# Optimization experiments

Hardware: AMD Instinct MI355X
Metric: run time of the kernel (lower is better)

The kernel has to match this reference:

```python
import jax, jax.numpy as jnp
import numpy as np

EPS = 1e-5

def setup_inputs() -> dict:
    key = jax.random.key(0)
    k1, k2, k3, k4, k5 = jax.random.split(key, 5)
    b, n, e, c = 256, 257, 768, 1
    x = jax.random.normal(k1, (b, n, e), dtype=jnp.float32)
    ln_gamma = jnp.ones((e,), dtype=jnp.float32)
    ln_beta = jnp.zeros((e,), dtype=jnp.float32)
    # nn.Linear default init: uniform(-1/sqrt(e), 1/sqrt(e))
    bound = 1.0 / np.sqrt(e)
    W = jax.random.uniform(k2, (c, e), dtype=jnp.float32, minval=-bound, maxval=bound)
    bias = jax.random.uniform(k3, (c,), dtype=jnp.float32, minval=-bound, maxval=bound)
    return {"x": x, "ln_gamma": ln_gamma, "ln_beta": ln_beta, "W": W, "bias": bias}

def reference(x, ln_gamma, ln_beta, W, bias):
    # drop CLS token: [b, n-1, e]
    h = x[:, 1:, :]
    mu = jnp.mean(h, axis=-1, keepdims=True)
    var = jnp.mean(jnp.square(h - mu), axis=-1, keepdims=True)
    h = (h - mu) * jax.lax.rsqrt(var + EPS) * ln_gamma + ln_beta
    # linear: [b, n-1, c]
    logits = jnp.einsum('bne,ce->bnc', h, W) + bias
    return jax.nn.sigmoid(logits)
```

## Files before the change

### kernel.cpp

```cpp
#include <hip/hip_runtime.h>
#include <hip/hip_bf16.h>

#define EPS 1e-5f

__global__ __launch_bounds__(256) void prep_kernel(
    const float* __restrict__ g, const float* __restrict__ beta,
    const float* __restrict__ W, const float* __restrict__ bias,
    float* __restrict__ gw, float* __restrict__ consts) {
    int t = threadIdx.x;
    float sgw = 0.f, sbw = 0.f;
    for (int i = t; i < 768; i += 256) {
        float gv = g[i] * W[i];
        gw[i] = gv;
        sgw += gv;
        sbw += beta[i] * W[i];
    }
    for (int m = 32; m; m >>= 1) {
        sgw += __shfl_xor(sgw, m);
        sbw += __shfl_xor(sbw, m);
    }
    __shared__ float red[8];
    int wid = t >> 6;
    if ((t & 63) == 0) { red[wid * 2] = sgw; red[wid * 2 + 1] = sbw; }
    __syncthreads();
    if (t == 0) {
        float a = red[0] + red[2] + red[4] + red[6];
        float b = red[1] + red[3] + red[5] + red[7];
        consts[0] = a;
        consts[1] = b + bias[0];
    }
}

__global__ __launch_bounds__(256) void head_kernel(
    const float* __restrict__ x, const float* __restrict__ gw,
    const float* __restrict__ consts, float* __restrict__ out) {
    const int lane = threadIdx.x & 63;
    const int wid  = threadIdx.x >> 6;
    const int row  = blockIdx.x * 4 + wid;
    const int b    = row >> 8;
    const int n    = row & 255;
    const float* __restrict__ xr = x + (size_t)(b * 257 + n + 1) * 768;

    float s1 = 0.f, s2 = 0.f, s3 = 0.f;
#pragma unroll
    for (int k = 0; k < 3; ++k) {
        int idx = (lane + k * 64) * 4;
        float4 v = *reinterpret_cast<const float4*>(xr + idx);
        float4 w = *reinterpret_cast<const float4*>(gw + idx);
        s1 += v.x + v.y + v.z + v.w;
        s2 += v.x * v.x + v.y * v.y + v.z * v.z + v.w * v.w;
        s3 += v.x * w.x + v.y * w.y + v.z * w.z + v.w * w.w;
    }
    for (int m = 32; m; m >>= 1) {
        s1 += __shfl_xor(s1, m);
        s2 += __shfl_xor(s2, m);
        s3 += __shfl_xor(s3, m);
    }
    if (lane == 0) {
        const float inv_e = 1.0f / 768.0f;
        float mu  = s1 * inv_e;
        float var = s2 * inv_e - mu * mu;
        float rs  = rsqrtf(var + EPS);
        float logit = rs * (s3 - mu * consts[0]) + consts[1];
        out[row] = 1.0f / (1.0f + __expf(-logit));
    }
}

extern "C" void kernel_launch(void* const* d_in, const int* in_sizes, int n_in,
                              void* d_out, int out_size, void* d_ws, size_t ws_size,
                              hipStream_t stream) {
    const float* x     = (const float*)d_in[0];
    const float* gamma = (const float*)d_in[1];
    const float* beta  = (const float*)d_in[2];
    const float* W     = (const float*)d_in[3];
    const float* bias  = (const float*)d_in[4];
    float* out = (float*)d_out;

    float* gw     = (float*)d_ws;
    float* consts = gw + 768;

    prep_kernel<<<1, 256, 0, stream>>>(gamma, beta, W, bias, gw, consts);

    const int rows = 256 * 256;
    head_kernel<<<rows / 4, 256, 0, stream>>>(x, gw, consts, out);
}
```

Before: 38.59 us.

## Fuse gamma*W prep into head kernel and process 16 rows per block

Removes the separate single-block prep kernel launch: each block now recomputes gamma*W and the two reduction constants into shared memory. Each wavefront now handles four rows using 16-lane groups with twelve float4 loads per lane, so the block covers 16 rows and the grid is four times smaller. This saves a launch and the serialization between the two kernels, at the cost of redundant per-block prep work, extra barriers and more loads in flight per lane.

```diff
diff --git a/kernel.cpp b/kernel.cpp
--- a/kernel.cpp
+++ b/kernel.cpp
@@ -3,65 +3,72 @@
 
 #define EPS 1e-5f
 
-__global__ __launch_bounds__(256) void prep_kernel(
-    const float* __restrict__ g, const float* __restrict__ beta,
-    const float* __restrict__ W, const float* __restrict__ bias,
-    float* __restrict__ gw, float* __restrict__ consts) {
-    int t = threadIdx.x;
-    float sgw = 0.f, sbw = 0.f;
-    for (int i = t; i < 768; i += 256) {
-        float gv = g[i] * W[i];
-        gw[i] = gv;
-        sgw += gv;
-        sbw += beta[i] * W[i];
+__global__ __launch_bounds__(256) void head_kernel(
+    const float* __restrict__ x, const float* __restrict__ gamma,
+    const float* __restrict__ beta, const float* __restrict__ W,
+    const float* __restrict__ bias, float* __restrict__ out) {
+    __shared__ float s_gw[768];
+    __shared__ float s_red[8];
+    __shared__ float s_c[2];
+
+    const int t = threadIdx.x;
+
+    {
+        float sgw = 0.f, sbw = 0.f;
+#pragma unroll
+        for (int i = t; i < 768; i += 256) {
+            float w  = W[i];
+            float gv = gamma[i] * w;
+            s_gw[i] = gv;
+            sgw += gv;
+            sbw += beta[i] * w;
+        }
+#pragma unroll
+        for (int m = 32; m; m >>= 1) {
+            sgw += __shfl_xor(sgw, m);
+            sbw += __shfl_xor(sbw, m);
+        }
+        const int wv = t >> 6;
+        if ((t & 63) == 0) { s_red[wv * 2] = sgw; s_red[wv * 2 + 1] = sbw; }
+        __syncthreads();
+        if (t == 0) {
+            s_c[0] = s_red[0] + s_red[2] + s_red[4] + s_red[6];
+            s_c[1] = s_red[1] + s_red[3] + s_red[5] + s_red[7] + bias[0];
+        }
+        __syncthreads();
     }
-    for (int m = 32; m; m >>= 1) {
-        sgw += __shfl_xor(sgw, m);
-        sbw += __shfl_xor(sbw, m);
-    }
-    __shared__ float red[8];
-    int wid = t >> 6;
-    if ((t & 63) == 0) { red[wid * 2] = sgw; red[wid * 2 + 1] = sbw; }
-    __syncthreads();
-    if (t == 0) {
-        float a = red[0] + red[2] + red[4] + red[6];
-        float b = red[1] + red[3] + red[5] + red[7];
-        consts[0] = a;
-        consts[1] = b + bias[0];
-    }
-}
 
-__global__ __launch_bounds__(256) void head_kernel(
-    const float* __restrict__ x, const float* __restrict__ gw,
-    const float* __restrict__ consts, float* __restrict__ out) {
-    const int lane = threadIdx.x & 63;
-    const int wid  = threadIdx.x >> 6;
-    const int row  = blockIdx.x * 4 + wid;
+    const int lane = t & 63;
+    const int wv   = t >> 6;
+    const int sl   = lane & 15;
+    const int grp  = lane >> 4;
+    const int row  = blockIdx.x * 16 + wv * 4 + grp;
     const int b    = row >> 8;
     const int n    = row & 255;
     const float* __restrict__ xr = x + (size_t)(b * 257 + n + 1) * 768;
 
     float s1 = 0.f, s2 = 0.f, s3 = 0.f;
 #pragma unroll
-    for (int k = 0; k < 3; ++k) {
-        int idx = (lane + k * 64) * 4;
+    for (int k = 0; k < 12; ++k) {
+        const int idx = sl * 4 + k * 64;
         float4 v = *reinterpret_cast<const float4*>(xr + idx);
-        float4 w = *reinterpret_cast<const float4*>(gw + idx);
+        float4 w = *reinterpret_cast<const float4*>(s_gw + idx);
         s1 += v.x + v.y + v.z + v.w;
         s2 += v.x * v.x + v.y * v.y + v.z * v.z + v.w * v.w;
         s3 += v.x * w.x + v.y * w.y + v.z * w.z + v.w * w.w;
     }
-    for (int m = 32; m; m >>= 1) {
+#pragma unroll
+    for (int m = 8; m; m >>= 1) {
         s1 += __shfl_xor(s1, m);
         s2 += __shfl_xor(s2, m);
         s3 += __shfl_xor(s3, m);
     }
-    if (lane == 0) {
+    if (sl == 0) {
         const float inv_e = 1.0f / 768.0f;
         float mu  = s1 * inv_e;
         float var = s2 * inv_e - mu * mu;
         float rs  = rsqrtf(var + EPS);
-        float logit = rs * (s3 - mu * consts[0]) + consts[1];
+        float logit = rs * (s3 - mu * s_c[0]) + s_c[1];
         out[row] = 1.0f / (1.0f + __expf(-logit));
     }
 }
@@ -76,11 +83,6 @@
     const float* bias  = (const float*)d_in[4];
     float* out = (float*)d_out;
 
-    float* gw     = (float*)d_ws;
-    float* consts = gw + 768;
-
-    prep_kernel<<<1, 256, 0, stream>>>(gamma, beta, W, bias, gw, consts);
-
     const int rows = 256 * 256;
-    head_kernel<<<rows / 4, 256, 0, stream>>>(x, gw, consts, out);
+    head_kernel<<<rows / 16, 256, 0, stream>>>(x, gamma, beta, W, bias, out);
 }
```

New measurement: 35.49 us, median of 2. 8.0% less time.
